# Kernel optimization log

Measured on AMD Instinct MI355X. Metric: run time of the kernel, lower is better.

The kernel has to match this reference:

```python
import jax, jax.numpy as jnp
import numpy as np

TEMPERATURE = 0.1  # init kwarg
EPS = 1e-8        # torch cosine_similarity eps


def setup_inputs() -> dict:
    key = jax.random.key(0)
    k1, k2, k3 = jax.random.split(key, 3)
    B, D, C = 4096, 1024, 32
    representations = jax.random.normal(k1, (B, D), dtype=jnp.float32)
    soft_labels = jax.random.uniform(k2, (B, C), dtype=jnp.float32)
    labels = jax.random.randint(k3, (B,), 0, 32, dtype=jnp.int64)
    return {
        "representations": representations,
        "soft_labels": soft_labels,
        "labels": labels,
        "pseudo_weight": 10,
    }


def reference(representations, soft_labels, labels, pseudo_weight):
    B = representations.shape[0]
    # row-normalize (cosine similarity)
    norms = jnp.maximum(jnp.linalg.norm(representations, axis=1, keepdims=True), EPS)
    rn = representations / norms
    Z = (rn @ rn.T) / TEMPERATURE                      # [B, B] scaled cosine sims
    E = jnp.exp(Z)
    off_diag = 1.0 - jnp.eye(B, dtype=Z.dtype)         # exclude j == i
    denom = jnp.sum(E * off_diag, axis=1, keepdims=True)   # [B, 1]
    loss_arr = -(Z - jnp.log(denom))                   # -log(exp(Z_ij)/denom_i)
    # positive-pair weights: same label, j != i (detached in original)
    pos = (labels[:, None] == labels[None, :]).astype(Z.dtype) * off_diag
    soft_sim = jax.lax.stop_gradient(soft_labels @ soft_labels.T)  # torch.inner, detached
    w = pos + pseudo_weight * soft_sim
    return jnp.sum(loss_arr * w) / B
```

## Files before the change

kernel.cpp:

```cpp
#include <hip/hip_runtime.h>
#include <hip/hip_bf16.h>
#include <stdint.h>


typedef float f32x4 __attribute__((ext_vector_type(4)));
typedef long i64;

#define INV_T 10.0f
#define Z_SCALE (INV_T / 256.0f)

#define CHUNK_STRIDE 262144

#define OFF_RNF8  0
#define OFF_DENOM 4194304
#define OFF_POSS  (OFF_DENOM + 16384)
#define OFF_G     (OFF_POSS + 16384)
#define OFF_OACC  (OFF_G + 131072)
#define OFF_DONE  (OFF_OACC + 16)
#define ZERO_SPAN 167936
#define OFF_CSP   (OFF_DENOM + ZERO_SPAN)
#define OFF_CCP   (OFF_CSP + 4096)
#define OFF_W     (OFF_CCP + 4096)

#define N_GEMM 528
#define N_G    512
#define N_W    16
#define N_ALL  (N_GEMM + N_G + N_W)

__global__ __launch_bounds__(256) void scl_stage1(const float* __restrict__ rep,
                                                  const float* __restrict__ sl,
                                                  const int* __restrict__ labels,
                                                  uint8_t* __restrict__ rnf8,
                                                  float* __restrict__ cs_part,
                                                  int* __restrict__ cc_part,
                                                  char* __restrict__ zbase) {
    int b = blockIdx.x;
    int t = threadIdx.x;
    if (b < 4096) {
        int row = b;
        const float4* src = reinterpret_cast<const float4*>(rep + (size_t)row * 1024);
        float4 v = src[t];
        float s = v.x * v.x + v.y * v.y + v.z * v.z + v.w * v.w;
#pragma unroll
        for (int m = 1; m < 64; m <<= 1) s += __shfl_xor(s, m, 64);
        __shared__ float red[4];
        if ((t & 63) == 0) red[t >> 6] = s;
        __syncthreads();
        s = red[0] + red[1] + red[2] + red[3];
        float nf = 16.0f / fmaxf(sqrtf(s), 1e-8f);
        int p = 0;
        p = __builtin_amdgcn_cvt_pk_fp8_f32(v.x * nf, v.y * nf, p, false);
        p = __builtin_amdgcn_cvt_pk_fp8_f32(v.z * nf, v.w * nf, p, true);
        *(uint32_t*)&rnf8[(size_t)(t >> 4) * CHUNK_STRIDE + row * 64 + (t & 15) * 4] =
            (uint32_t)p;
    } else if (b < 4128) {
        __shared__ float part[8][32];
        __shared__ int bins[32];
        int bb = b - 4096;
        if (t < 32) bins[t] = 0;
        __syncthreads();
        if (t < 128) atomicAdd(&bins[labels[bb * 128 + t]], 1);
        int c = t & 31, rg = t >> 5;
        float s = 0.f;
#pragma unroll 4
        for (int k = 0; k < 16; ++k) {
            int i = bb * 128 + rg * 16 + k;
            s += sl[i * 32 + c];
        }
        part[rg][c] = s;
        __syncthreads();
        if (t < 32) {
            float tot = 0.f;
#pragma unroll
            for (int g = 0; g < 8; ++g) tot += part[g][t];
            cs_part[bb * 32 + t] = tot;
            cc_part[bb * 32 + t] = bins[t];
        }
    } else {
        int zb = b - 4128;
        *(uint4*)(zbase + (size_t)zb * 4096 + t * 16) = (uint4){0, 0, 0, 0};
    }
}

__global__ __launch_bounds__(256) void scl_main(const uint8_t* __restrict__ rnf8,
                                                const float* __restrict__ sl,
                                                const int* __restrict__ labels,
                                                const float* __restrict__ cs_part,
                                                const int* __restrict__ cc_part,
                                                const int* __restrict__ pwp,
                                                float* __restrict__ denom,
                                                float* __restrict__ posS,
                                                float* __restrict__ G,
                                                float* __restrict__ W) {
    int tid = threadIdx.x;
    int bIdx = blockIdx.x;

    if (bIdx >= N_GEMM) {
        if (bIdx < N_GEMM + N_G) {
            __shared__ __align__(16) uint8_t rns[128 * 64];
            __shared__ __align__(16) float sls[128 * 32];
            int idx = bIdx - N_GEMM;
            int dblk = idx & 15, ks = idx >> 4;
            int i0 = ks * 128;
            const uint8_t* slab = rnf8 + (size_t)dblk * CHUNK_STRIDE + (size_t)i0 * 64;
#pragma unroll
            for (int p = 0; p < 2; ++p) {
                int off = p * 4096 + tid * 16;
                *(uint4*)&rns[off] = *(const uint4*)&slab[off];
            }
#pragma unroll
            for (int p = 0; p < 4; ++p) {
                int off = p * 1024 + tid * 4;
                *(float4*)&sls[off] = *(const float4*)&sl[(size_t)i0 * 32 + off];
            }
            __syncthreads();
            int dq = tid >> 5, c = tid & 31;
            int d0 = dblk * 64 + dq * 8;
            float acc[8];
#pragma unroll
            for (int j = 0; j < 8; ++j) acc[j] = 0.f;
#pragma unroll 4
            for (int k = 0; k < 128; ++k) {
                uint2 rv = *(const uint2*)&rns[k * 64 + dq * 8];
                float sv = sls[k * 32 + c];
                acc[0] += __builtin_amdgcn_cvt_f32_fp8((int)rv.x, 0) * sv;
                acc[1] += __builtin_amdgcn_cvt_f32_fp8((int)rv.x, 1) * sv;
                acc[2] += __builtin_amdgcn_cvt_f32_fp8((int)rv.x, 2) * sv;
                acc[3] += __builtin_amdgcn_cvt_f32_fp8((int)rv.x, 3) * sv;
                acc[4] += __builtin_amdgcn_cvt_f32_fp8((int)rv.y, 0) * sv;
                acc[5] += __builtin_amdgcn_cvt_f32_fp8((int)rv.y, 1) * sv;
                acc[6] += __builtin_amdgcn_cvt_f32_fp8((int)rv.y, 2) * sv;
                acc[7] += __builtin_amdgcn_cvt_f32_fp8((int)rv.y, 3) * sv;
            }
#pragma unroll
            for (int j = 0; j < 8; ++j)
                atomicAdd(&G[(d0 + j) * 32 + c], acc[j] * 0.0625f);
        } else {
            __shared__ __align__(16) float css[32];
            __shared__ int ccs[32];
            if (tid < 32) {
                float s = 0.f; int n = 0;
#pragma unroll
                for (int b = 0; b < 32; ++b) { s += cs_part[b * 32 + tid]; n += cc_part[b * 32 + tid]; }
                css[tid] = s; ccs[tid] = n;
            }
            __syncthreads();
            int bits = *pwp;
            float pw = (bits >= -(1 << 22) && bits <= (1 << 22)) ? (float)bits
                                                                 : __int_as_float(bits);
            int i = (bIdx - (N_GEMM + N_G)) * 256 + tid;
            const f32x4* sl4 = (const f32x4*)sl;
            const f32x4* cs4 = (const f32x4*)css;
            float dW = 0.f;
#pragma unroll
            for (int q = 0; q < 8; ++q) {
                f32x4 s = sl4[i * 8 + q];
                f32x4 c = cs4[q];
                dW += s[0] * c[0] + s[1] * c[1] + s[2] * c[2] + s[3] * c[3];
            }
            W[i] = (float)(ccs[labels[i]] - 1) + pw * dW;
        }
        return;
    }

    __shared__ int lblA[128], lblB[128];

    int L = (bIdx & 7) * 66 + (bIdx >> 3);
    int bi = 0, rem = L;
    while (rem >= 32 - bi) { rem -= 32 - bi; ++bi; }
    int bj = bi + rem;
    int rowA0 = bi * 128, colB0 = bj * 128;

    if (tid < 128) {
        lblA[tid] = labels[rowA0 + tid];
        lblB[tid] = labels[colB0 + tid];
    }
    __syncthreads();

    int lane = tid & 63, warp = tid >> 6;
    int wr = warp >> 1, wc = warp & 1;
    int m_ = lane & 15, g = lane >> 4;

    const uint8_t* gAf = rnf8 + (size_t)(rowA0 + wr * 64 + m_) * 64 + g * 16;
    const uint8_t* gBf = rnf8 + (size_t)(colB0 + wc * 64 + m_) * 64 + g * 16;

    f32x4 acc[4][4];
#pragma unroll
    for (int a = 0; a < 4; ++a)
#pragma unroll
        for (int b = 0; b < 4; ++b) acc[a][b] = (f32x4){0.f, 0.f, 0.f, 0.f};

    f32x4 a0[4], b0[4], a1[4], b1[4], a2[4], b2[4];

#define MFMA_SET(AF, BF)                                                       \
    _Pragma("unroll") for (int s = 0; s < 2; ++s)                              \
        _Pragma("unroll") for (int ti = 0; ti < 4; ++ti)                       \
            _Pragma("unroll") for (int tj = 0; tj < 4; ++tj) {                 \
                i64 av = ((const i64*)&AF[ti])[s];                             \
                i64 bv = ((const i64*)&BF[tj])[s];                             \
                acc[ti][tj] = __builtin_amdgcn_mfma_f32_16x16x32_fp8_fp8(      \
                    av, bv, acc[ti][tj], 0, 0, 0);                             \
            }
#define LOADF(AF, BF, KT)                                                      \
    {                                                                          \
        size_t co = (size_t)(KT) * CHUNK_STRIDE;                               \
        _Pragma("unroll") for (int t = 0; t < 4; ++t) {                        \
            AF[t] = *(const f32x4*)(gAf + co + t * 1024);                      \
            BF[t] = *(const f32x4*)(gBf + co + t * 1024);                      \
        }                                                                      \
    }

    LOADF(a0, b0, 0)
    LOADF(a1, b1, 1)
    LOADF(a2, b2, 2)
    MFMA_SET(a0, b0) LOADF(a0, b0, 3)
    MFMA_SET(a1, b1) LOADF(a1, b1, 4)
    MFMA_SET(a2, b2) LOADF(a2, b2, 5)
    MFMA_SET(a0, b0) LOADF(a0, b0, 6)
    MFMA_SET(a1, b1) LOADF(a1, b1, 7)
    MFMA_SET(a2, b2) LOADF(a2, b2, 8)
    MFMA_SET(a0, b0) LOADF(a0, b0, 9)
    MFMA_SET(a1, b1) LOADF(a1, b1, 10)
    MFMA_SET(a2, b2) LOADF(a2, b2, 11)
    MFMA_SET(a0, b0) LOADF(a0, b0, 12)
    MFMA_SET(a1, b1) LOADF(a1, b1, 13)
    MFMA_SET(a2, b2) LOADF(a2, b2, 14)
    MFMA_SET(a0, b0) LOADF(a0, b0, 15)
    MFMA_SET(a1, b1)
    MFMA_SET(a2, b2)
    MFMA_SET(a0, b0)
#undef LOADF
#undef MFMA_SET

    bool isDiag = (bi == bj);
    int cl = m_;
    float colE[4] = {0.f, 0.f, 0.f, 0.f}, colP[4] = {0.f, 0.f, 0.f, 0.f};
#pragma unroll
    for (int ti = 0; ti < 4; ++ti) {
        int rowLoc = wr * 64 + ti * 16 + g * 4;
        float rE[4] = {0.f, 0.f, 0.f, 0.f}, rP[4] = {0.f, 0.f, 0.f, 0.f};
        int lr[4];
#pragma unroll
        for (int r = 0; r < 4; ++r) lr[r] = lblA[rowLoc + r];
#pragma unroll
        for (int tj = 0; tj < 4; ++tj) {
            int colLoc = wc * 64 + tj * 16 + cl;
            int gCol = colB0 + colLoc;
            int lc = lblB[colLoc];
            f32x4 a = acc[ti][tj];
#pragma unroll
            for (int r = 0; r < 4; ++r) {
                int gRow = rowA0 + rowLoc + r;
                float z = Z_SCALE * a[r];
                float e = __expf(z);
                bool offd = (gRow != gCol);
                if (!offd) e = 0.f;
                rE[r] += e;
                colE[tj] += e;
                if (offd && (lr[r] == lc)) { rP[r] += z; colP[tj] += z; }
            }
        }
#pragma unroll
        for (int r = 0; r < 4; ++r) {
            float v = rE[r], p = rP[r];
#pragma unroll
            for (int msk = 1; msk < 16; msk <<= 1) {
                v += __shfl_xor(v, msk, 64);
                p += __shfl_xor(p, msk, 64);
            }
            if (cl == 0) {
                int gRow = rowA0 + rowLoc + r;
                atomicAdd(&denom[gRow], v);
                atomicAdd(&posS[gRow], p);
            }
        }
    }
    if (!isDiag) {
#pragma unroll
        for (int tj = 0; tj < 4; ++tj) {
            float v = colE[tj], p = colP[tj];
            v += __shfl_xor(v, 16, 64); p += __shfl_xor(p, 16, 64);
            v += __shfl_xor(v, 32, 64); p += __shfl_xor(p, 32, 64);
            if (g == 0) {
                int gCol = colB0 + wc * 64 + tj * 16 + cl;
                atomicAdd(&denom[gCol], v);
                atomicAdd(&posS[gCol], p);
            }
        }
    }
}

__global__ __launch_bounds__(256) void scl_finalize(const float* __restrict__ denom,
                                                    const float* __restrict__ posS,
                                                    const float* __restrict__ W,
                                                    const float* __restrict__ G,
                                                    const int* __restrict__ pwp,
                                                    double* __restrict__ oacc,
                                                    int* __restrict__ done,
                                                    float* __restrict__ out) {
    int t = threadIdx.x;
    __shared__ double wsum[4];
    double contrib = 0.0;

    if (blockIdx.x < 8) {
        int i0 = blockIdx.x * 512 + t;
        float t0 = __logf(denom[i0]) * W[i0] - posS[i0];
        float t1 = __logf(denom[i0 + 256]) * W[i0 + 256] - posS[i0 + 256];
        double td = (double)t0 + (double)t1;
#pragma unroll
        for (int m = 1; m < 64; m <<= 1) td += __shfl_xor(td, m, 64);
        if ((t & 63) == 0) wsum[t >> 6] = td;
        __syncthreads();
        contrib = wsum[0] + wsum[1] + wsum[2] + wsum[3];
    } else {
        int bits = *pwp;
        float pw = (bits >= -(1 << 22) && bits <= (1 << 22)) ? (float)bits
                                                             : __int_as_float(bits);
        const f32x4* G4 = (const f32x4*)G;
        float gs = 0.f;
#pragma unroll
        for (int q = 0; q < 32; ++q) {
            f32x4 v = G4[q * 256 + t];
            gs += v[0] * v[0] + v[1] * v[1] + v[2] * v[2] + v[3] * v[3];
        }
        double gd = (double)gs;
#pragma unroll
        for (int m = 1; m < 64; m <<= 1) gd += __shfl_xor(gd, m, 64);
        if ((t & 63) == 0) wsum[t >> 6] = gd;
        __syncthreads();
        contrib = -(double)(pw * INV_T) * (wsum[0] + wsum[1] + wsum[2] + wsum[3]);
    }

    if (t == 0) {
        atomicAdd(oacc, contrib);
        __threadfence();
        int old = atomicAdd(done, 1);
        if (old == 8) {
            double tot = atomicAdd(oacc, 0.0);
            out[0] = (float)(tot * (1.0 / 4096.0));
        }
    }
}

extern "C" void kernel_launch(void* const* d_in, const int* in_sizes, int n_in,
                              void* d_out, int out_size, void* d_ws, size_t ws_size,
                              hipStream_t stream) {
    const float* rep = (const float*)d_in[0];
    const float* sl = (const float*)d_in[1];
    const int* labels = (const int*)d_in[2];
    const int* pwp = (const int*)d_in[3];

    char* ws = (char*)d_ws;
    uint8_t* rnf8 = (uint8_t*)(ws + OFF_RNF8);
    float* denom = (float*)(ws + OFF_DENOM);
    float* posS = (float*)(ws + OFF_POSS);
    float* G = (float*)(ws + OFF_G);
    double* oacc = (double*)(ws + OFF_OACC);
    int* done = (int*)(ws + OFF_DONE);
    float* cs_part = (float*)(ws + OFF_CSP);
    int* cc_part = (int*)(ws + OFF_CCP);
    float* W = (float*)(ws + OFF_W);

    scl_stage1<<<4169, 256, 0, stream>>>(rep, sl, labels, rnf8,
                                         cs_part, cc_part, ws + OFF_DENOM);
    scl_main<<<N_ALL, 256, 0, stream>>>(rnf8, sl, labels, cs_part, cc_part, pwp,
                                        denom, posS, G, W);
    scl_finalize<<<9, 256, 0, stream>>>(denom, posS, W, G, pwp, oacc, done,
                                        (float*)d_out);
}
```

Baseline: 116.1 us.

## Widen symmetric GEMM tiles to 128x256 and shrink to two-stage register pipeline

Each GEMM block now covers a 128-row by 256-column strip of the upper triangle instead of a 128x128 tile, with each warp computing 64x128. This roughly halves the number of GEMM blocks and raises per-warp reuse of A fragments. Warps whose 128-column half falls below the diagonal return early. The unrolled triple-buffered fragment prefetch is replaced by a double-buffered loop, and doubling the accumulators raises register pressure, which may lower occupancy and leave some warps idle.

```diff
diff --git a/kernel.cpp b/kernel.cpp
--- a/kernel.cpp
+++ b/kernel.cpp
@@ -22,7 +22,7 @@
 #define OFF_CCP   (OFF_CSP + 4096)
 #define OFF_W     (OFF_CCP + 4096)
 
-#define N_GEMM 528
+#define N_GEMM 272
 #define N_G    512
 #define N_W    16
 #define N_ALL  (N_GEMM + N_G + N_W)
@@ -163,39 +163,41 @@
         return;
     }
 
-    __shared__ int lblA[128], lblB[128];
-
-    int L = (bIdx & 7) * 66 + (bIdx >> 3);
+    __shared__ int lblA[128], lblB[256];
+
+    int L = (bIdx & 7) * 34 + (bIdx >> 3);
     int bi = 0, rem = L;
-    while (rem >= 32 - bi) { rem -= 32 - bi; ++bi; }
-    int bj = bi + rem;
-    int rowA0 = bi * 128, colB0 = bj * 128;
-
-    if (tid < 128) {
-        lblA[tid] = labels[rowA0 + tid];
-        lblB[tid] = labels[colB0 + tid];
-    }
+    while (rem >= 16 - (bi >> 1)) { rem -= 16 - (bi >> 1); ++bi; }
+    int bjp = (bi >> 1) + rem;
+    int rowA0 = bi * 128, colB0 = bjp * 256;
+
+    if (tid < 128) lblA[tid] = labels[rowA0 + tid];
+    lblB[tid] = labels[colB0 + tid];
     __syncthreads();
 
     int lane = tid & 63, warp = tid >> 6;
     int wr = warp >> 1, wc = warp & 1;
     int m_ = lane & 15, g = lane >> 4;
 
+    int cb = 2 * bjp + wc;
+    if (cb < bi) return;
+    bool diagStrip = (cb == bi);
+
     const uint8_t* gAf = rnf8 + (size_t)(rowA0 + wr * 64 + m_) * 64 + g * 16;
-    const uint8_t* gBf = rnf8 + (size_t)(colB0 + wc * 64 + m_) * 64 + g * 16;
-
-    f32x4 acc[4][4];
+    const uint8_t* gBf = rnf8 + (size_t)(colB0 + wc * 128 + m_) * 64 + g * 16;
+
+    f32x4 acc[4][8];
 #pragma unroll
     for (int a = 0; a < 4; ++a)
 #pragma unroll
-        for (int b = 0; b < 4; ++b) acc[a][b] = (f32x4){0.f, 0.f, 0.f, 0.f};
-
-    f32x4 a0[4], b0[4], a1[4], b1[4], a2[4], b2[4];
+        for (int b = 0; b < 8; ++b) acc[a][b] = (f32x4){0.f, 0.f, 0.f, 0.f};
+
+    f32x4 a0[4], b0[8], a1[4], b1[8];
 
 #define MFMA_SET(AF, BF)                                                       \
     _Pragma("unroll") for (int s = 0; s < 2; ++s)                              \
         _Pragma("unroll") for (int ti = 0; ti < 4; ++ti)                       \
-            _Pragma("unroll") for (int tj = 0; tj < 4; ++tj) {                 \
+            _Pragma("unroll") for (int tj = 0; tj < 8; ++tj) {                 \
                 i64 av = ((const i64*)&AF[ti])[s];                             \
                 i64 bv = ((const i64*)&BF[tj])[s];                             \
                 acc[ti][tj] = __builtin_amdgcn_mfma_f32_16x16x32_fp8_fp8(      \
@@ -204,37 +206,25 @@
 #define LOADF(AF, BF, KT)                                                      \
     {                                                                          \
         size_t co = (size_t)(KT) * CHUNK_STRIDE;                               \
-        _Pragma("unroll") for (int t = 0; t < 4; ++t) {                        \
+        _Pragma("unroll") for (int t = 0; t < 4; ++t)                          \
             AF[t] = *(const f32x4*)(gAf + co + t * 1024);                      \
+        _Pragma("unroll") for (int t = 0; t < 8; ++t)                          \
             BF[t] = *(const f32x4*)(gBf + co + t * 1024);                      \
-        }                                                                      \
     }
 
     LOADF(a0, b0, 0)
-    LOADF(a1, b1, 1)
-    LOADF(a2, b2, 2)
-    MFMA_SET(a0, b0) LOADF(a0, b0, 3)
-    MFMA_SET(a1, b1) LOADF(a1, b1, 4)
-    MFMA_SET(a2, b2) LOADF(a2, b2, 5)
-    MFMA_SET(a0, b0) LOADF(a0, b0, 6)
-    MFMA_SET(a1, b1) LOADF(a1, b1, 7)
-    MFMA_SET(a2, b2) LOADF(a2, b2, 8)
-    MFMA_SET(a0, b0) LOADF(a0, b0, 9)
-    MFMA_SET(a1, b1) LOADF(a1, b1, 10)
-    MFMA_SET(a2, b2) LOADF(a2, b2, 11)
-    MFMA_SET(a0, b0) LOADF(a0, b0, 12)
-    MFMA_SET(a1, b1) LOADF(a1, b1, 13)
-    MFMA_SET(a2, b2) LOADF(a2, b2, 14)
-    MFMA_SET(a0, b0) LOADF(a0, b0, 15)
-    MFMA_SET(a1, b1)
-    MFMA_SET(a2, b2)
-    MFMA_SET(a0, b0)
+    for (int kt = 0; kt < 16; kt += 2) {
+        LOADF(a1, b1, kt + 1)
+        MFMA_SET(a0, b0)
+        if (kt + 2 < 16) LOADF(a0, b0, kt + 2)
+        MFMA_SET(a1, b1)
+    }
 #undef LOADF
 #undef MFMA_SET
 
-    bool isDiag = (bi == bj);
     int cl = m_;
-    float colE[4] = {0.f, 0.f, 0.f, 0.f}, colP[4] = {0.f, 0.f, 0.f, 0.f};
+    float colE[8] = {0.f, 0.f, 0.f, 0.f, 0.f, 0.f, 0.f, 0.f};
+    float colP[8] = {0.f, 0.f, 0.f, 0.f, 0.f, 0.f, 0.f, 0.f};
 #pragma unroll
     for (int ti = 0; ti < 4; ++ti) {
         int rowLoc = wr * 64 + ti * 16 + g * 4;
@@ -243,8 +233,8 @@
 #pragma unroll
         for (int r = 0; r < 4; ++r) lr[r] = lblA[rowLoc + r];
 #pragma unroll
-        for (int tj = 0; tj < 4; ++tj) {
-            int colLoc = wc * 64 + tj * 16 + cl;
+        for (int tj = 0; tj < 8; ++tj) {
+            int colLoc = wc * 128 + tj * 16 + cl;
             int gCol = colB0 + colLoc;
             int lc = lblB[colLoc];
             f32x4 a = acc[ti][tj];
@@ -275,14 +265,14 @@
             }
         }
     }
-    if (!isDiag) {
-#pragma unroll
-        for (int tj = 0; tj < 4; ++tj) {
+    if (!diagStrip) {
+#pragma unroll
+        for (int tj = 0; tj < 8; ++tj) {
             float v = colE[tj], p = colP[tj];
             v += __shfl_xor(v, 16, 64); p += __shfl_xor(p, 16, 64);
             v += __shfl_xor(v, 32, 64); p += __shfl_xor(p, 32, 64);
             if (g == 0) {
-                int gCol = colB0 + wc * 64 + tj * 16 + cl;
+                int gCol = colB0 + wc * 128 + tj * 16 + cl;
                 atomicAdd(&denom[gCol], v);
                 atomicAdd(&posS[gCol], p);
             }
```

Measured after the change: 121.7 us. 1.05x slower.
